# Kernel tuning notes

Hardware: AMD Instinct MI355X
Metric: run time of the kernel (lower is better)

The kernel has to match this reference:

```python
import jax, jax.numpy as jnp
import numpy as np

N = 16384       # pedestrian_num
D_IN = 2        # input_size
H = 64          # hidden_size


def setup_inputs() -> dict:
    key = jax.random.key(0)
    ks = jax.random.split(key, 4)
    data = jax.random.normal(ks[0], (N, D_IN), dtype=jnp.float32)
    # Linear weights stored as [in, out]; scaled like torch default init (~1/sqrt(in)).
    W1 = jax.random.normal(ks[1], (D_IN, 32), dtype=jnp.float32) / np.sqrt(D_IN)
    b1 = jnp.zeros((32,), dtype=jnp.float32)
    W2 = jax.random.normal(ks[2], (32, 64), dtype=jnp.float32) / np.sqrt(32)
    b2 = jnp.zeros((64,), dtype=jnp.float32)
    W3 = jax.random.normal(ks[3], (64, H), dtype=jnp.float32) / np.sqrt(64)
    b3 = jnp.zeros((H,), dtype=jnp.float32)
    return {"data": data, "W1": W1, "b1": b1, "W2": W2, "b2": b2, "W3": W3, "b3": b3}


def reference(data, W1, b1, W2, b2, W3, b3):
    # Per-pedestrian MLP (batched over all N pedestrians at once).
    h = jax.nn.relu(data @ W1 + b1)          # [N, 32]
    h = jax.nn.relu(h @ W2 + b2)             # [N, 64]
    h = h @ W3 + b3                          # [N, H]
    # Spatial affinity: the original fills the lower triangle with <h_i, h_j>
    # and its softmax reads entry [max(i,j), min(i,j)], i.e. the full
    # symmetric Gram matrix G = h @ h.T.
    G = jnp.einsum("nd,md->nm", h, h)        # [N, N], symmetric
    # Row-wise softmax over the symmetric affinity matrix.
    return jax.nn.softmax(G, axis=-1)
```

## Files before the change

### kernel.cpp

```cpp
#include <hip/hip_runtime.h>

#define N     16384
#define DH    64
#define TILE  128
#define NT    (N / TILE)
#define S2    133

typedef __attribute__((ext_vector_type(8))) short  short8;
typedef __attribute__((ext_vector_type(4))) float  f32x4;

__device__ __forceinline__ ushort bf_hi(float x) {
    unsigned u = __float_as_uint(x);
    unsigned r = u + 0x7FFFu + ((u >> 16) & 1u);
    return (ushort)(r >> 16);
}
__device__ __forceinline__ float bf_val(ushort h) {
    return __uint_as_float(((unsigned)h) << 16);
}

__device__ __forceinline__ short8 ldfrag(const ushort* __restrict__ p, int row, int koff) {
    return *(const short8*)(p + (size_t)row * DH + koff);
}

__global__ __launch_bounds__(128) void mlp_kernel(
    const float* __restrict__ data,
    const float* __restrict__ W1, const float* __restrict__ b1,
    const float* __restrict__ W2, const float* __restrict__ b2,
    const float* __restrict__ W3, const float* __restrict__ b3,
    ushort* __restrict__ hHi, ushort* __restrict__ hLo)
{
    __shared__ float sW1[64], sb1[32], sW2[32 * 64], sb2[64], sW3[64 * 64], sb3[64];
    const int tid = threadIdx.x;
    if (tid < 64) sW1[tid] = W1[tid];
    if (tid < 32) sb1[tid] = b1[tid];
    if (tid < 64) sb2[tid] = b2[tid];
    if (tid < 64) sb3[tid] = b3[tid];
    for (int t = tid; t < 32 * 64; t += 128) sW2[t] = W2[t];
    for (int t = tid; t < 64 * 64; t += 128) sW3[t] = W3[t];
    __syncthreads();

    const int i = blockIdx.x * 128 + tid;
    const float x0 = data[2 * i + 0];
    const float x1 = data[2 * i + 1];

    float h1[32];
#pragma unroll
    for (int o = 0; o < 32; ++o)
        h1[o] = fmaxf(0.f, fmaf(x0, sW1[o], fmaf(x1, sW1[32 + o], sb1[o])));

    float h2[64];
#pragma unroll
    for (int o = 0; o < 64; ++o) {
        float a = sb2[o];
#pragma unroll
        for (int k = 0; k < 32; ++k) a = fmaf(h1[k], sW2[k * 64 + o], a);
        h2[o] = fmaxf(0.f, a);
    }

    ushort hs[64], ls[64];
#pragma unroll
    for (int o = 0; o < 64; ++o) {
        float a = sb3[o];
#pragma unroll
        for (int k = 0; k < 64; ++k) a = fmaf(h2[k], sW3[k * 64 + o], a);
        const ushort hb = bf_hi(a);
        hs[o] = hb;
        ls[o] = bf_hi(a - bf_val(hb));
    }
#pragma unroll
    for (int q = 0; q < 8; ++q) {
        short8 vh, vl;
#pragma unroll
        for (int t = 0; t < 8; ++t) { vh[t] = (short)hs[q * 8 + t]; vl[t] = (short)ls[q * 8 + t]; }
        *(short8*)(hHi + (size_t)i * DH + q * 8) = vh;
        *(short8*)(hLo + (size_t)i * DH + q * 8) = vl;
    }
}

__device__ __forceinline__ void stage_B(
    const ushort* __restrict__ hHi, const ushort* __restrict__ hLo,
    int brow0, int tid, ushort* __restrict__ sB)
{
    const int arr = tid >> 7;
    const int r   = tid & 127;
    const ushort* __restrict__ src = (arr ? hLo : hHi) + (size_t)(brow0 + r) * DH;
    ushort* __restrict__ dst = sB + arr * (TILE * DH) + r * 64;
    const int sw = (r & 7);
#pragma unroll
    for (int q = 0; q < 8; ++q) {
        const short8 v = *(const short8*)(src + q * 8);
        *(short8*)(dst + 8 * (q ^ sw)) = v;
    }
}

__device__ __forceinline__ short8 ldB(const ushort* __restrict__ sB,
                                      int arr, int row, int ks, int kb)
{
    return *(const short8*)(sB + arr * (TILE * DH) + row * 64 + 8 * (((ks << 2) + kb) ^ (row & 7)));
}

__device__ __forceinline__ void gram_tile(
    const ushort* __restrict__ hHi, const ushort* __restrict__ hLo,
    const ushort* __restrict__ sB,
    int bi, int wave, int r16, int kb, f32x4 acc[2][8])
{
#pragma unroll
    for (int rb = 0; rb < 2; ++rb)
#pragma unroll
        for (int cb = 0; cb < 8; ++cb) acc[rb][cb] = (f32x4){0.f, 0.f, 0.f, 0.f};

    const int arow = bi * TILE + wave * 16 + r16;
#pragma unroll
    for (int ks = 0; ks < 2; ++ks) {
        const int koff = ks * 32 + kb * 8;
        const short8 Ah0 = ldfrag(hHi, arow,      koff);
        const short8 Ah1 = ldfrag(hHi, arow + 64, koff);
        const short8 Al0 = ldfrag(hLo, arow,      koff);
        const short8 Al1 = ldfrag(hLo, arow + 64, koff);
#pragma unroll
        for (int cb = 0; cb < 8; ++cb) {
            const int brow = cb * 16 + r16;
            const short8 Bh = ldB(sB, 0, brow, ks, kb);
            const short8 Bl = ldB(sB, 1, brow, ks, kb);
            acc[0][cb] = __builtin_amdgcn_mfma_f32_16x16x32_bf16(Ah0, Bh, acc[0][cb], 0, 0, 0);
            acc[0][cb] = __builtin_amdgcn_mfma_f32_16x16x32_bf16(Ah0, Bl, acc[0][cb], 0, 0, 0);
            acc[0][cb] = __builtin_amdgcn_mfma_f32_16x16x32_bf16(Al0, Bh, acc[0][cb], 0, 0, 0);
            acc[1][cb] = __builtin_amdgcn_mfma_f32_16x16x32_bf16(Ah1, Bh, acc[1][cb], 0, 0, 0);
            acc[1][cb] = __builtin_amdgcn_mfma_f32_16x16x32_bf16(Ah1, Bl, acc[1][cb], 0, 0, 0);
            acc[1][cb] = __builtin_amdgcn_mfma_f32_16x16x32_bf16(Al1, Bh, acc[1][cb], 0, 0, 0);
        }
    }
}

__device__ __forceinline__ int tile_row(int wave, int kb, int rb, int reg) {
    return rb * 64 + wave * 16 + kb * 4 + reg;
}

__global__ __launch_bounds__(256, 2) void pass1_mfma(
    const ushort* __restrict__ hHi, const ushort* __restrict__ hLo,
    float* __restrict__ part_m, float* __restrict__ part_l)
{
    const int bj = blockIdx.x, c = blockIdx.y;
    if (16 * c > bj) return;
    const int bi_end = min(16 * c + 16, bj + 1);

    __shared__ __attribute__((aligned(16))) ushort sB[2 * TILE * DH];
    __shared__ float jm[4 * 128], jl[4 * 128];

    const int tid = threadIdx.x;
    const int wave = tid >> 6, lane = tid & 63;
    const int r16 = lane & 15, kb = lane >> 4;

    stage_B(hHi, hLo, bj * TILE, tid, sB);
    __syncthreads();

    for (int bi = 16 * c; bi < bi_end; ++bi) {
        f32x4 acc[2][8];
        gram_tile(hHi, hLo, sB, bi, wave, r16, kb, acc);

#pragma unroll
        for (int rb = 0; rb < 2; ++rb) {
#pragma unroll
            for (int e = 0; e < 4; ++e) {
                float m = acc[rb][0][e];
#pragma unroll
                for (int cb = 1; cb < 8; ++cb) m = fmaxf(m, acc[rb][cb][e]);
                m = fmaxf(m, __shfl_xor(m, 1));
                m = fmaxf(m, __shfl_xor(m, 2));
                m = fmaxf(m, __shfl_xor(m, 4));
                m = fmaxf(m, __shfl_xor(m, 8));
                float s = 0.f;
#pragma unroll
                for (int cb = 0; cb < 8; ++cb) s += __expf(acc[rb][cb][e] - m);
                s += __shfl_xor(s, 1);
                s += __shfl_xor(s, 2);
                s += __shfl_xor(s, 4);
                s += __shfl_xor(s, 8);
                if (r16 == 0) {
                    const int grow = bi * TILE + tile_row(wave, kb, rb, e);
                    part_m[(size_t)bj * N + grow] = m;
                    part_l[(size_t)bj * N + grow] = s;
                }
            }
        }

        if (bi != bj) {
#pragma unroll
            for (int cb = 0; cb < 8; ++cb) {
                float m = acc[0][cb][0];
#pragma unroll
                for (int rb = 0; rb < 2; ++rb)
#pragma unroll
                    for (int e = 0; e < 4; ++e) m = fmaxf(m, acc[rb][cb][e]);
                m = fmaxf(m, __shfl_xor(m, 16));
                m = fmaxf(m, __shfl_xor(m, 32));
                float s = 0.f;
#pragma unroll
                for (int rb = 0; rb < 2; ++rb)
#pragma unroll
                    for (int e = 0; e < 4; ++e) s += __expf(acc[rb][cb][e] - m);
                s += __shfl_xor(s, 16);
                s += __shfl_xor(s, 32);
                if (kb == 0) { jm[wave * 128 + cb * 16 + r16] = m; jl[wave * 128 + cb * 16 + r16] = s; }
            }
            __syncthreads();
            if (tid < 128) {
                float M = jm[tid];
#pragma unroll
                for (int w = 1; w < 4; ++w) M = fmaxf(M, jm[w * 128 + tid]);
                float L = 0.f;
#pragma unroll
                for (int w = 0; w < 4; ++w) L += jl[w * 128 + tid] * __expf(jm[w * 128 + tid] - M);
                part_m[(size_t)bi * N + bj * TILE + tid] = M;
                part_l[(size_t)bi * N + bj * TILE + tid] = L;
            }
            __syncthreads();
        }
    }
}

__global__ __launch_bounds__(256) void merge_kernel(
    const float* __restrict__ part_m, const float* __restrict__ part_l,
    float* __restrict__ srow)
{
    const int i = blockIdx.x * 256 + threadIdx.x;
    float M = -3.0e38f;
    for (int o = 0; o < NT; ++o) M = fmaxf(M, part_m[(size_t)o * N + i]);
    float L = 0.f;
    for (int o = 0; o < NT; ++o)
        L = fmaf(part_l[(size_t)o * N + i], __expf(part_m[(size_t)o * N + i] - M), L);
    srow[i] = M + __logf(L);
}

__global__ __launch_bounds__(256, 2) void pass2_mfma(
    const ushort* __restrict__ hHi, const ushort* __restrict__ hLo,
    const float* __restrict__ srow,
    float* __restrict__ out)
{
    const int p = blockIdx.x;
    const int xcd = p & 7, slot = p >> 3;
    const int bj  = xcd * 16 + (slot & 15);
    const int bi0 = (slot >> 4) * 16;

    const int tid = threadIdx.x;
    const int wave = tid >> 6, lane = tid & 63;
    const int r16 = lane & 15, kb = lane >> 4;

    __shared__ __attribute__((aligned(16))) ushort sB[2 * TILE * DH];
    __shared__ float ldsP[64 * S2];

    stage_B(hHi, hLo, bj * TILE, tid, sB);
    __syncthreads();

    for (int it = 0; it < 16; ++it) {
        const int bi = bi0 + it;

        f32x4 acc[2][8];
        gram_tile(hHi, hLo, sB, bi, wave, r16, kb, acc);

#pragma unroll
        for (int hh = 0; hh < 2; ++hh) {
#pragma unroll
            for (int reg = 0; reg < 4; ++reg) {
                const int rl   = wave * 16 + kb * 4 + reg;
                const int grow = bi * TILE + hh * 64 + rl;
                const float s  = srow[grow];
#pragma unroll
                for (int cb = 0; cb < 8; ++cb)
                    ldsP[rl * S2 + cb * 16 + r16] = __expf(acc[hh][cb][reg] - s);
            }
            __syncthreads();
#pragma unroll
            for (int qq = 0; qq < 8; ++qq) {
                const int f4 = tid + 256 * qq;
                const int rl = f4 >> 5, c4 = f4 & 31;
                const f32x4 v = *(const f32x4*)&ldsP[rl * S2 + c4 * 4];
                f32x4* dst = (f32x4*)(out + (size_t)(bi * TILE + hh * 64 + rl) * N + bj * TILE + c4 * 4);
                __builtin_nontemporal_store(v, dst);
            }
            __syncthreads();
        }
    }
}

extern "C" void kernel_launch(void* const* d_in, const int* in_sizes, int n_in,
                              void* d_out, int out_size, void* d_ws, size_t ws_size,
                              hipStream_t stream)
{
    const float* data = (const float*)d_in[0];
    const float* W1   = (const float*)d_in[1];
    const float* b1   = (const float*)d_in[2];
    const float* W2   = (const float*)d_in[3];
    const float* b2   = (const float*)d_in[4];
    const float* W3   = (const float*)d_in[5];
    const float* b3   = (const float*)d_in[6];
    float* out = (float*)d_out;

    float* part_m = (float*)d_ws;
    float* part_l = part_m + (size_t)NT * N;
    float* srow   = part_l + (size_t)NT * N;
    ushort* hHi   = (ushort*)(srow + 2 * N);
    ushort* hLo   = hHi + (size_t)N * DH;

    mlp_kernel<<<N / 128, 128, 0, stream>>>(data, W1, b1, W2, b2, W3, b3, hHi, hLo);
    pass1_mfma<<<dim3(NT, 8), 256, 0, stream>>>(hHi, hLo, part_m, part_l);
    merge_kernel<<<N / 256, 256, 0, stream>>>(part_m, part_l, srow);
    pass2_mfma<<<1024, 256, 0, stream>>>(hHi, hLo, srow, out);
}
```

Measured before the change: 396.3 us.

## Flatten pass1 to one block per triangular tile and make pass2 staging per-wave

Pass1 now launches one block per upper-triangular tile pair. A balanced triangle decode pairs short and long columns and groups them by XCD, replacing the variable-length loop over bi per (bj, chunk) block that left many blocks empty. Shared memory is aliased between the B tile and the reduction scratch, and the launch bound is raised to 4 blocks per CU to increase occupancy, at the cost of restaging B for every tile. Pass2 gives each wave its own 16-row LDS staging buffer, so the block-wide syncthreads around the output store are removed.

```diff
diff --git a/kernel.cpp b/kernel.cpp
--- a/kernel.cpp
+++ b/kernel.cpp
@@ -136,16 +136,27 @@
     return rb * 64 + wave * 16 + kb * 4 + reg;
 }
 
-__global__ __launch_bounds__(256, 2) void pass1_mfma(
+__device__ __forceinline__ void tri_decode(int p, int& bi, int& bj) {
+    const int xcd = p & 7, s = p >> 3;
+    const int q = s / 129, r = s % 129;
+    const int P = xcd * 8 + q;
+    if (r <= P) { bi = r;         bj = P;       }
+    else        { bi = r - P - 1; bj = 127 - P; }
+}
+
+#define SMEM1_BYTES 32768
+
+__global__ __launch_bounds__(256, 4) void pass1_mfma(
     const ushort* __restrict__ hHi, const ushort* __restrict__ hLo,
     float* __restrict__ part_m, float* __restrict__ part_l)
 {
-    const int bj = blockIdx.x, c = blockIdx.y;
-    if (16 * c > bj) return;
-    const int bi_end = min(16 * c + 16, bj + 1);
-
-    __shared__ __attribute__((aligned(16))) ushort sB[2 * TILE * DH];
-    __shared__ float jm[4 * 128], jl[4 * 128];
+    int bi, bj;
+    tri_decode(blockIdx.x, bi, bj);
+
+    __shared__ __attribute__((aligned(16))) char smem[SMEM1_BYTES];
+    ushort* sB = (ushort*)smem;
+    float*  jm = (float*)smem;
+    float*  jl = jm + 512;
 
     const int tid = threadIdx.x;
     const int wave = tid >> 6, lane = tid & 63;
@@ -154,67 +165,65 @@
     stage_B(hHi, hLo, bj * TILE, tid, sB);
     __syncthreads();
 
-    for (int bi = 16 * c; bi < bi_end; ++bi) {
-        f32x4 acc[2][8];
-        gram_tile(hHi, hLo, sB, bi, wave, r16, kb, acc);
-
-#pragma unroll
-        for (int rb = 0; rb < 2; ++rb) {
-#pragma unroll
-            for (int e = 0; e < 4; ++e) {
-                float m = acc[rb][0][e];
-#pragma unroll
-                for (int cb = 1; cb < 8; ++cb) m = fmaxf(m, acc[rb][cb][e]);
-                m = fmaxf(m, __shfl_xor(m, 1));
-                m = fmaxf(m, __shfl_xor(m, 2));
-                m = fmaxf(m, __shfl_xor(m, 4));
-                m = fmaxf(m, __shfl_xor(m, 8));
-                float s = 0.f;
-#pragma unroll
-                for (int cb = 0; cb < 8; ++cb) s += __expf(acc[rb][cb][e] - m);
-                s += __shfl_xor(s, 1);
-                s += __shfl_xor(s, 2);
-                s += __shfl_xor(s, 4);
-                s += __shfl_xor(s, 8);
-                if (r16 == 0) {
-                    const int grow = bi * TILE + tile_row(wave, kb, rb, e);
-                    part_m[(size_t)bj * N + grow] = m;
-                    part_l[(size_t)bj * N + grow] = s;
-                }
+    f32x4 acc[2][8];
+    gram_tile(hHi, hLo, sB, bi, wave, r16, kb, acc);
+
+#pragma unroll
+    for (int rb = 0; rb < 2; ++rb) {
+#pragma unroll
+        for (int e = 0; e < 4; ++e) {
+            float m = acc[rb][0][e];
+#pragma unroll
+            for (int cb = 1; cb < 8; ++cb) m = fmaxf(m, acc[rb][cb][e]);
+            m = fmaxf(m, __shfl_xor(m, 1));
+            m = fmaxf(m, __shfl_xor(m, 2));
+            m = fmaxf(m, __shfl_xor(m, 4));
+            m = fmaxf(m, __shfl_xor(m, 8));
+            float s = 0.f;
+#pragma unroll
+            for (int cb = 0; cb < 8; ++cb) s += __expf(acc[rb][cb][e] - m);
+            s += __shfl_xor(s, 1);
+            s += __shfl_xor(s, 2);
+            s += __shfl_xor(s, 4);
+            s += __shfl_xor(s, 8);
+            if (r16 == 0) {
+                const int grow = bi * TILE + tile_row(wave, kb, rb, e);
+                part_m[(size_t)bj * N + grow] = m;
+                part_l[(size_t)bj * N + grow] = s;
             }
         }
-
-        if (bi != bj) {
-#pragma unroll
-            for (int cb = 0; cb < 8; ++cb) {
-                float m = acc[0][cb][0];
-#pragma unroll
-                for (int rb = 0; rb < 2; ++rb)
-#pragma unroll
-                    for (int e = 0; e < 4; ++e) m = fmaxf(m, acc[rb][cb][e]);
-                m = fmaxf(m, __shfl_xor(m, 16));
-                m = fmaxf(m, __shfl_xor(m, 32));
-                float s = 0.f;
-#pragma unroll
-                for (int rb = 0; rb < 2; ++rb)
-#pragma unroll
-                    for (int e = 0; e < 4; ++e) s += __expf(acc[rb][cb][e] - m);
-                s += __shfl_xor(s, 16);
-                s += __shfl_xor(s, 32);
-                if (kb == 0) { jm[wave * 128 + cb * 16 + r16] = m; jl[wave * 128 + cb * 16 + r16] = s; }
-            }
-            __syncthreads();
-            if (tid < 128) {
-                float M = jm[tid];
-#pragma unroll
-                for (int w = 1; w < 4; ++w) M = fmaxf(M, jm[w * 128 + tid]);
-                float L = 0.f;
-#pragma unroll
-                for (int w = 0; w < 4; ++w) L += jl[w * 128 + tid] * __expf(jm[w * 128 + tid] - M);
-                part_m[(size_t)bi * N + bj * TILE + tid] = M;
-                part_l[(size_t)bi * N + bj * TILE + tid] = L;
-            }
-            __syncthreads();
+    }
+
+    if (bi != bj) {
+        __syncthreads();
+#pragma unroll
+        for (int cb = 0; cb < 8; ++cb) {
+            float m = acc[0][cb][0];
+#pragma unroll
+            for (int rb = 0; rb < 2; ++rb)
+#pragma unroll
+                for (int e = 0; e < 4; ++e) m = fmaxf(m, acc[rb][cb][e]);
+            m = fmaxf(m, __shfl_xor(m, 16));
+            m = fmaxf(m, __shfl_xor(m, 32));
+            float s = 0.f;
+#pragma unroll
+            for (int rb = 0; rb < 2; ++rb)
+#pragma unroll
+                for (int e = 0; e < 4; ++e) s += __expf(acc[rb][cb][e] - m);
+            s += __shfl_xor(s, 16);
+            s += __shfl_xor(s, 32);
+            if (kb == 0) { jm[wave * 128 + cb * 16 + r16] = m; jl[wave * 128 + cb * 16 + r16] = s; }
+        }
+        __syncthreads();
+        if (tid < 128) {
+            float M = jm[tid];
+#pragma unroll
+            for (int w = 1; w < 4; ++w) M = fmaxf(M, jm[w * 128 + tid]);
+            float L = 0.f;
+#pragma unroll
+            for (int w = 0; w < 4; ++w) L += jl[w * 128 + tid] * __expf(jm[w * 128 + tid] - M);
+            part_m[(size_t)bi * N + bj * TILE + tid] = M;
+            part_l[(size_t)bi * N + bj * TILE + tid] = L;
         }
     }
 }
@@ -247,11 +256,13 @@
     const int r16 = lane & 15, kb = lane >> 4;
 
     __shared__ __attribute__((aligned(16))) ushort sB[2 * TILE * DH];
-    __shared__ float ldsP[64 * S2];
+    __shared__ float ldsP[4][16 * S2];
 
     stage_B(hHi, hLo, bj * TILE, tid, sB);
     __syncthreads();
 
+    float* __restrict__ myP = &ldsP[wave][0];
+
     for (int it = 0; it < 16; ++it) {
         const int bi = bi0 + it;
 
@@ -262,23 +273,22 @@
         for (int hh = 0; hh < 2; ++hh) {
 #pragma unroll
             for (int reg = 0; reg < 4; ++reg) {
-                const int rl   = wave * 16 + kb * 4 + reg;
-                const int grow = bi * TILE + hh * 64 + rl;
+                const int rl16 = kb * 4 + reg;
+                const int grow = bi * TILE + hh * 64 + wave * 16 + rl16;
                 const float s  = srow[grow];
 #pragma unroll
                 for (int cb = 0; cb < 8; ++cb)
-                    ldsP[rl * S2 + cb * 16 + r16] = __expf(acc[hh][cb][reg] - s);
+                    myP[rl16 * S2 + cb * 16 + r16] = __expf(acc[hh][cb][reg] - s);
             }
-            __syncthreads();
-#pragma unroll
-            for (int qq = 0; qq < 8; ++qq) {
-                const int f4 = tid + 256 * qq;
-                const int rl = f4 >> 5, c4 = f4 & 31;
-                const f32x4 v = *(const f32x4*)&ldsP[rl * S2 + c4 * 4];
-                f32x4* dst = (f32x4*)(out + (size_t)(bi * TILE + hh * 64 + rl) * N + bj * TILE + c4 * 4);
+#pragma unroll
+            for (int q = 0; q < 8; ++q) {
+                const int f4 = lane + 64 * q;
+                const int rl16 = f4 >> 5, c4 = f4 & 31;
+                const f32x4 v = *(const f32x4*)&myP[rl16 * S2 + c4 * 4];
+                f32x4* dst = (f32x4*)(out + (size_t)(bi * TILE + hh * 64 + wave * 16 + rl16) * N
+                                      + bj * TILE + c4 * 4);
                 __builtin_nontemporal_store(v, dst);
             }
-            __syncthreads();
         }
     }
 }
@@ -303,7 +313,7 @@
     ushort* hLo   = hHi + (size_t)N * DH;
 
     mlp_kernel<<<N / 128, 128, 0, stream>>>(data, W1, b1, W2, b2, W3, b3, hHi, hLo);
-    pass1_mfma<<<dim3(NT, 8), 256, 0, stream>>>(hHi, hLo, part_m, part_l);
+    pass1_mfma<<<NT * (NT + 1) / 2, 256, 0, stream>>>(hHi, hLo, part_m, part_l);
     merge_kernel<<<N / 256, 256, 0, stream>>>(part_m, part_l, srow);
     pass2_mfma<<<1024, 256, 0, stream>>>(hHi, hLo, srow, out);
 }
```

Measured after the change: 364.6 us. -8.0%, faster.
